# Kernel tuning notes

Measured on AMD Instinct MI355X. Metric: run time of the kernel, lower is better.

The kernel has to match this reference:

```python
import jax, jax.numpy as jnp
import numpy as np

NUM_HEADS = 12
WINDOW = 7            # window_size (and window_pretrain)
MASK_WINDOWS = 64     # windows per image (56x56 feature map / 7x7 windows)
TABLE_SIZE = (2 * WINDOW - 1) ** 2  # 169


def setup_inputs() -> dict:
    key = jax.random.key(0)
    ks = jax.random.split(key, 8)
    B, L, C = 2048, WINDOW * WINDOW, 384
    x = jax.random.normal(ks[0], (B, L, C), jnp.float32)
    rel_index = jax.random.randint(ks[1], (L * L,), 0, TABLE_SIZE, jnp.int32)
    attn_mask = jax.random.normal(ks[2], (1, MASK_WINDOWS, 1, L, L), jnp.float32) * 0.05
    # learned params
    qkv_w = jax.random.normal(ks[3], (C, 3 * C), jnp.float32) * 0.02
    qkv_b = jnp.zeros((3 * C,), jnp.float32)
    rel_bias_table = jax.random.normal(ks[4], (TABLE_SIZE, NUM_HEADS), jnp.float32) * 0.02
    proj_w = jax.random.normal(ks[5], (C, C), jnp.float32) * 0.02
    proj_b = jnp.zeros((C,), jnp.float32)
    return {"x": x, "rel_index": rel_index, "attn_mask": attn_mask,
            "qkv_w": qkv_w, "qkv_b": qkv_b, "rel_bias_table": rel_bias_table,
            "proj_w": proj_w, "proj_b": proj_b}


def reference(x, rel_index, attn_mask, qkv_w, qkv_b, rel_bias_table, proj_w, proj_b):
    B, L, C = x.shape
    H = NUM_HEADS
    D = C // H
    scale = D ** -0.5
    # qkv projection -> [3, B, H, L, D]
    qkv = (x @ qkv_w + qkv_b).reshape(B, L, 3, H, D).transpose(2, 0, 3, 1, 4)
    q, k, v = qkv[0], qkv[1], qkv[2]
    attn = jnp.einsum('bhqd,bhkd->bhqk', q * scale, k)  # [B,H,L,L]
    # gathered relative position bias: [L*L, H] -> [H, L, L]
    bias = rel_bias_table[rel_index].reshape(L, L, H).transpose(2, 0, 1)
    attn = attn + bias[None]
    # shifted-window mask add (with_mask=True path)
    attn = attn.reshape(-1, MASK_WINDOWS, H, L, L) + attn_mask
    attn = attn.reshape(-1, H, L, L)
    attn = jax.nn.softmax(attn, axis=-1)
    out = jnp.einsum('bhqk,bhkd->bqhd', attn, v).reshape(B, L, C)
    return out @ proj_w + proj_b
```

## Files before the change

kernel.cpp:

```cpp
#include <hip/hip_runtime.h>

typedef _Float16 half8 __attribute__((ext_vector_type(8)));
typedef float f32x4 __attribute__((ext_vector_type(4)));

constexpr int NB = 2048;
constexpr int CDIM = 384;
constexpr int NH = 12;
constexpr int MM = NB * 49;
constexpr int NTOT = 1152;
constexpr float SCALE = 0.17677669529663687f;

constexpr int XBLK = 37632;
constexpr int WBLK = 2304;

__device__ __forceinline__ void async16(const void* g, void* l) {
    __builtin_amdgcn_global_load_lds((const __attribute__((address_space(1))) void*)g,
                                     (__attribute__((address_space(3))) void*)l, 16, 0, 0);
}


__global__ __launch_bounds__(256) void prep(const float* __restrict__ x,
                                            const float* __restrict__ qkv_w,
                                            const float* __restrict__ proj_w,
                                            const int* __restrict__ rel_index,
                                            const float* __restrict__ rtable,
                                            const float* __restrict__ mask,
                                            _Float16* __restrict__ x_h,
                                            _Float16* __restrict__ qkvT,
                                            _Float16* __restrict__ projT,
                                            float* __restrict__ FT) {
    int bid = blockIdx.x;
    if (bid < XBLK) {
        size_t i = ((size_t)bid * 256 + threadIdx.x) * 4;
        float4 v = *(const float4*)(x + i);
        _Float16 h0 = (_Float16)v.x, h1 = (_Float16)v.y, h2 = (_Float16)v.z, h3 = (_Float16)v.w;
        _Float16* o = x_h + i;
        o[0] = h0; o[1] = h1; o[2] = h2; o[3] = h3;
    } else if (bid < XBLK + WBLK) {
        int i = (bid - XBLK) * 256 + threadIdx.x;
        if (i < 1152 * 384) {
            int n = i / 384, kk = i % 384;
            qkvT[i] = (_Float16)qkv_w[kk * 1152 + n];
        } else {
            int j = i - 1152 * 384;
            int n = j / 384, kk = j % 384;
            projT[j] = (_Float16)proj_w[kk * 384 + n];
        }
    } else {
        int wh = bid - XBLK - WBLK;
        int w = wh / 12, h = wh - w * 12;
        float* dst = FT + (size_t)wh * 4096;
        for (int idx = threadIdx.x; idx < 4096; idx += 256) {
            int k = idx >> 6, q = idx & 63;
            float v = 0.f;
            if (k < 49 && q < 49)
                v = rtable[rel_index[q * 49 + k] * NH + h] + mask[(size_t)w * 2401 + q * 49 + k];
            dst[idx] = v;
        }
    }
}


__global__ __launch_bounds__(256) void gemm_qkv(const _Float16* __restrict__ A,
                                                const _Float16* __restrict__ Bt,
                                                const float* __restrict__ qkv_b,
                                                _Float16* __restrict__ C) {
    __shared__ union {
        struct { _Float16 A[128 * 64]; _Float16 B[128 * 64]; } st;
        _Float16 tile[128 * 136];
    } sm;
    _Float16* As = sm.st.A;
    _Float16* Bs = sm.st.B;

    const int K = 384;
    const int tn = blockIdx.x, tm = blockIdx.y;
    const int t = threadIdx.x;
    const int wave = t >> 6, lane = t & 63;
    const int wm = (wave & 1) * 64, wn = (wave >> 1) * 64;
    const int quad = lane >> 4, l16 = lane & 15;
    const int rsub = lane >> 3, p = lane & 7;

    f32x4 acc[4][4] = {};
    const _Float16* Abase = A + (size_t)(tm * 128) * K;
    const _Float16* Bbase = Bt + (size_t)(tn * 128) * K;

    for (int k0 = 0; k0 < K; k0 += 64) {
        __syncthreads();
#pragma unroll
        for (int n = 0; n < 4; n++) {
            int ni = wave * 4 + n;
            int row = ni * 8 + rsub;
            int chunk = p ^ (row & 7);
            async16(Abase + (size_t)row * K + k0 + chunk * 8, (char*)As + ni * 1024);
            async16(Bbase + (size_t)row * K + k0 + chunk * 8, (char*)Bs + ni * 1024);
        }
        __syncthreads();
#pragma unroll
        for (int ks = 0; ks < 2; ks++) {
            half8 af[4], bfv[4];
#pragma unroll
            for (int i = 0; i < 4; i++)
                af[i] = *(const half8*)(&As[(wm + i * 16 + l16) * 64 + (((ks * 4 + quad) ^ (l16 & 7)) * 8)]);
#pragma unroll
            for (int j = 0; j < 4; j++)
                bfv[j] = *(const half8*)(&Bs[(wn + j * 16 + l16) * 64 + (((ks * 4 + quad) ^ (l16 & 7)) * 8)]);
#pragma unroll
            for (int i = 0; i < 4; i++)
#pragma unroll
                for (int j = 0; j < 4; j++)
                    acc[i][j] = __builtin_amdgcn_mfma_f32_16x16x32_f16(af[i], bfv[j], acc[i][j], 0, 0, 0);
        }
    }

    __syncthreads();
    const int nbase = tn * 128, mbase = tm * 128;
    const float s = (tn < 3) ? SCALE : 1.f;
    float bj[4];
#pragma unroll
    for (int j = 0; j < 4; j++) bj[j] = qkv_b[nbase + wn + j * 16 + l16];

#pragma unroll
    for (int j = 0; j < 4; j++) {
        int n = wn + j * 16 + l16;
#pragma unroll
        for (int i = 0; i < 4; i++) {
#pragma unroll
            for (int r = 0; r < 4; r++) {
                int m = wm + i * 16 + quad * 4 + r;
                sm.tile[m * 136 + n] = (_Float16)((acc[i][j][r] + bj[j]) * s);
            }
        }
    }
    __syncthreads();

    const int rcol = (t & 15) * 8;
    const int rrow0 = t >> 4;
#pragma unroll
    for (int g = 0; g < 8; g++) {
        int row = g * 16 + rrow0;
        half8 val = *(const half8*)(&sm.tile[row * 136 + rcol]);
        *(half8*)(C + (size_t)(mbase + row) * NTOT + nbase + rcol) = val;
    }
}


__global__ __launch_bounds__(256) void attn_kernel(const _Float16* __restrict__ C,
                                                   const float* __restrict__ FT,
                                                   _Float16* __restrict__ out) {
    __shared__ _Float16 Vt[4][32 * 72];
    __shared__ _Float16 Pb[4][16 * 72];
    const int t = threadIdx.x;
    const int wave = t >> 6, lane = t & 63, quad = lane >> 4, l16 = lane & 15;
    const int gw = blockIdx.x * 4 + wave;
    const int b = gw / 12, h = gw - b * 12;

    const _Float16* qb = C + (size_t)b * 49 * NTOT + h * 32;
    const _Float16* kb = qb + 384;
    const _Float16* vb = qb + 768;
    const float* Fb = FT + ((size_t)((b & 63) * 12 + h)) * 4096;

    _Float16* vt = Vt[wave];
    {
        int d = lane >> 1, seg = lane & 1;
        half8 z = {};
        *(half8*)(&vt[d * 72 + 48 + seg * 8]) = z;
    }
#pragma unroll
    for (int i2 = 0; i2 < 4; i2++) {
        int l = i2 * 16 + (lane >> 2);
        int d0 = (lane & 3) * 8;
        if (l < 49) {
            half8 v8 = *(const half8*)(vb + (size_t)l * NTOT + d0);
#pragma unroll
            for (int e = 0; e < 8; e++)
                vt[(d0 + e) * 72 + l] = v8[e];
        }
    }

    half8 bk[4];
#pragma unroll
    for (int j = 0; j < 4; j++) {
        int krow = j * 16 + l16; if (krow > 48) krow = 48;
        bk[j] = *(const half8*)(kb + (size_t)krow * NTOT + quad * 8);
    }
    half8 bv[2][2];
#pragma unroll
    for (int nt = 0; nt < 2; nt++)
#pragma unroll
        for (int ks = 0; ks < 2; ks++)
            bv[nt][ks] = *(const half8*)(&vt[(nt * 16 + l16) * 72 + ks * 32 + quad * 8]);

    _Float16* Pw = Pb[wave];
#pragma unroll
    for (int i = 0; i < 4; i++) {
        int qrow = i * 16 + l16; if (qrow > 48) qrow = 48;
        half8 aq = *(const half8*)(qb + (size_t)qrow * NTOT + quad * 8);

        f32x4 acc[4];
#pragma unroll
        for (int j = 0; j < 4; j++)
            acc[j] = *(const f32x4*)(Fb + (j * 16 + l16) * 64 + i * 16 + quad * 4);
#pragma unroll
        for (int j = 0; j < 4; j++)
            acc[j] = __builtin_amdgcn_mfma_f32_16x16x32_f16(aq, bk[j], acc[j], 0, 0, 0);

        if (l16 != 0) {
#pragma unroll
            for (int r = 0; r < 4; r++) acc[3][r] = -1e30f;
        }

        float rinv[4];
#pragma unroll
        for (int r = 0; r < 4; r++) {
            float m = fmaxf(fmaxf(acc[0][r], acc[1][r]), fmaxf(acc[2][r], acc[3][r]));
            m = fmaxf(m, __shfl_xor(m, 1, 64));
            m = fmaxf(m, __shfl_xor(m, 2, 64));
            m = fmaxf(m, __shfl_xor(m, 4, 64));
            m = fmaxf(m, __shfl_xor(m, 8, 64));
            float sum = 0.f;
#pragma unroll
            for (int j = 0; j < 4; j++) {
                float e = __expf(acc[j][r] - m);
                acc[j][r] = e;
                sum += e;
            }
            sum += __shfl_xor(sum, 1, 64);
            sum += __shfl_xor(sum, 2, 64);
            sum += __shfl_xor(sum, 4, 64);
            sum += __shfl_xor(sum, 8, 64);
            rinv[r] = 1.f / sum;
        }

#pragma unroll
        for (int j = 0; j < 4; j++)
#pragma unroll
            for (int r = 0; r < 4; r++)
                Pw[(quad * 4 + r) * 72 + j * 16 + l16] = (_Float16)acc[j][r];

        f32x4 oacc[2] = {};
#pragma unroll
        for (int ks = 0; ks < 2; ks++) {
            half8 ap = *(const half8*)(&Pw[l16 * 72 + ks * 32 + quad * 8]);
#pragma unroll
            for (int nt = 0; nt < 2; nt++)
                oacc[nt] = __builtin_amdgcn_mfma_f32_16x16x32_f16(ap, bv[nt][ks], oacc[nt], 0, 0, 0);
        }

#pragma unroll
        for (int nt = 0; nt < 2; nt++)
#pragma unroll
            for (int r = 0; r < 4; r++) {
                int q = i * 16 + quad * 4 + r;
                if (q < 49)
                    out[((size_t)b * 49 + q) * CDIM + h * 32 + nt * 16 + l16] =
                        (_Float16)(oacc[nt][r] * rinv[r]);
            }
    }
}


__global__ __launch_bounds__(256) void gemm_proj(const _Float16* __restrict__ A,
                                                 const _Float16* __restrict__ Bt,
                                                 const float* __restrict__ proj_b,
                                                 float* __restrict__ out) {
    __shared__ _Float16 As[128 * 64];
    __shared__ _Float16 Bs[128 * 64];
    const int K = 384;
    const int tn = blockIdx.x, tm = blockIdx.y;
    const int t = threadIdx.x;
    const int wave = t >> 6, lane = t & 63;
    const int wm = (wave & 1) * 64, wn = (wave >> 1) * 64;
    const int quad = lane >> 4, l16 = lane & 15;
    const int rsub = lane >> 3, p = lane & 7;

    f32x4 acc[4][4] = {};
    const _Float16* Abase = A + (size_t)(tm * 128) * K;
    const _Float16* Bbase = Bt + (size_t)(tn * 128) * K;

    for (int k0 = 0; k0 < K; k0 += 64) {
        __syncthreads();
#pragma unroll
        for (int n = 0; n < 4; n++) {
            int ni = wave * 4 + n;
            int row = ni * 8 + rsub;
            int chunk = p ^ (row & 7);
            async16(Abase + (size_t)row * K + k0 + chunk * 8, (char*)As + ni * 1024);
            async16(Bbase + (size_t)row * K + k0 + chunk * 8, (char*)Bs + ni * 1024);
        }
        __syncthreads();
#pragma unroll
        for (int ks = 0; ks < 2; ks++) {
            half8 af[4], bfv[4];
#pragma unroll
            for (int i = 0; i < 4; i++)
                af[i] = *(const half8*)(&As[(wm + i * 16 + l16) * 64 + (((ks * 4 + quad) ^ (l16 & 7)) * 8)]);
#pragma unroll
            for (int j = 0; j < 4; j++)
                bfv[j] = *(const half8*)(&Bs[(wn + j * 16 + l16) * 64 + (((ks * 4 + quad) ^ (l16 & 7)) * 8)]);
#pragma unroll
            for (int i = 0; i < 4; i++)
#pragma unroll
                for (int j = 0; j < 4; j++)
                    acc[i][j] = __builtin_amdgcn_mfma_f32_16x16x32_f16(af[i], bfv[j], acc[i][j], 0, 0, 0);
        }
    }

    const int mbase = tm * 128, nbase = tn * 128;
#pragma unroll
    for (int j = 0; j < 4; j++) {
        int n = nbase + wn + j * 16 + l16;
        float bias = proj_b[n];
#pragma unroll
        for (int i = 0; i < 4; i++) {
#pragma unroll
            for (int r = 0; r < 4; r++) {
                int m = mbase + wm + i * 16 + quad * 4 + r;
                out[(size_t)m * CDIM + n] = acc[i][j][r] + bias;
            }
        }
    }
}


extern "C" void kernel_launch(void* const* d_in, const int* in_sizes, int n_in,
                              void* d_out, int out_size, void* d_ws, size_t ws_size,
                              hipStream_t stream) {
    const float* x        = (const float*)d_in[0];
    const int*   rel_idx  = (const int*)d_in[1];
    const float* amask    = (const float*)d_in[2];
    const float* qkv_w    = (const float*)d_in[3];
    const float* qkv_b    = (const float*)d_in[4];
    const float* rtable   = (const float*)d_in[5];
    const float* proj_w   = (const float*)d_in[6];
    const float* proj_b   = (const float*)d_in[7];
    float* out = (float*)d_out;

    char* w = (char*)d_ws;
    const size_t XB = (size_t)MM * CDIM * 2;
    const size_t CB = (size_t)MM * NTOT * 2;
    _Float16* x_h    = (_Float16*)w;
    _Float16* wqkvT  = (_Float16*)(w + XB);
    _Float16* wprojT = (_Float16*)(w + XB + 884736);
    _Float16* Cbuf   = (_Float16*)(w + XB + 884736 + 294912);
    float*    FT     = (float*)(w + XB + 884736 + 294912 + CB);
    _Float16* ao_h   = x_h;

    prep<<<XBLK + WBLK + 768, 256, 0, stream>>>(x, qkv_w, proj_w, rel_idx, rtable, amask,
                                                x_h, wqkvT, wprojT, FT);
    gemm_qkv<<<dim3(9, MM / 128), 256, 0, stream>>>(x_h, wqkvT, qkv_b, Cbuf);
    attn_kernel<<<NB * NH / 4, 256, 0, stream>>>(Cbuf, FT, ao_h);
    gemm_proj<<<dim3(3, MM / 128), 256, 0, stream>>>(ao_h, wprojT, proj_b, out);
}
```

Baseline: 625.8 us.

## Fuse QKV projection with window attention per window, remap proj GEMM blocks

Replaces the separate QKV GEMM and attention kernels with one kernel per window. It loads the 49x384 input tile into LDS, computes Q/K/V for three heads per wave pair with MFMA, and runs softmax attention directly from LDS. This removes the round trip of the large fp16 QKV intermediate through global memory. The cost is that weights are read from global/L2 per window with low reuse, LDS use is high, and the padded 64-row tile reads past the last window (handled by padding the workspace). The projection GEMM also gets a 1D grid with a chunked block remap, probably for XCD/L2 locality.

```diff
diff --git a/kernel.cpp b/kernel.cpp
--- a/kernel.cpp
+++ b/kernel.cpp
@@ -7,11 +7,13 @@
 constexpr int CDIM = 384;
 constexpr int NH = 12;
 constexpr int MM = NB * 49;
-constexpr int NTOT = 1152;
 constexpr float SCALE = 0.17677669529663687f;
 
 constexpr int XBLK = 37632;
 constexpr int WBLK = 2304;
+
+constexpr int PROJ_BLOCKS = 3 * (MM / 128);
+constexpr int PROJ_CHUNK  = PROJ_BLOCKS / 8;
 
 __device__ __forceinline__ void async16(const void* g, void* l) {
     __builtin_amdgcn_global_load_lds((const __attribute__((address_space(1))) void*)g,
@@ -61,200 +63,158 @@
 }
 
 
-__global__ __launch_bounds__(256) void gemm_qkv(const _Float16* __restrict__ A,
-                                                const _Float16* __restrict__ Bt,
-                                                const float* __restrict__ qkv_b,
-                                                _Float16* __restrict__ C) {
-    __shared__ union {
-        struct { _Float16 A[128 * 64]; _Float16 B[128 * 64]; } st;
-        _Float16 tile[128 * 136];
-    } sm;
-    _Float16* As = sm.st.A;
-    _Float16* Bs = sm.st.B;
-
-    const int K = 384;
-    const int tn = blockIdx.x, tm = blockIdx.y;
+__global__ __launch_bounds__(512, 2) void qkv_attn(const _Float16* __restrict__ x_h,
+                                                   const _Float16* __restrict__ qkvT,
+                                                   const float* __restrict__ qkv_b,
+                                                   const float* __restrict__ FT,
+                                                   _Float16* __restrict__ ao) {
+    __shared__ _Float16 xs[64 * 384];
+    __shared__ _Float16 Qs[4][64 * 40];
+    __shared__ _Float16 Ks[4][64 * 40];
+    __shared__ _Float16 Vt[4][32 * 72];
+    __shared__ _Float16 Pb[8][16 * 72];
+
+    const int b = blockIdx.x;
     const int t = threadIdx.x;
     const int wave = t >> 6, lane = t & 63;
-    const int wm = (wave & 1) * 64, wn = (wave >> 1) * 64;
     const int quad = lane >> 4, l16 = lane & 15;
-    const int rsub = lane >> 3, p = lane & 7;
-
-    f32x4 acc[4][4] = {};
-    const _Float16* Abase = A + (size_t)(tm * 128) * K;
-    const _Float16* Bbase = Bt + (size_t)(tn * 128) * K;
-
-    for (int k0 = 0; k0 < K; k0 += 64) {
+    const int gsel = wave >> 1, p = wave & 1;
+
+    const _Float16* xw = x_h + (size_t)b * 49 * 384;
+#pragma unroll
+    for (int rnd = 0; rnd < 6; rnd++) {
+        int g = rnd * 512 + t;
+        int row = g / 48, c = g - row * 48;
+        int cs = c ^ (row & 7);
+        async16(xw + row * 384 + cs * 8, (char*)xs + (rnd * 8192 + wave * 1024));
+    }
+    __syncthreads();
+
+    _Float16* Qg = Qs[gsel];
+    _Float16* Kg = Ks[gsel];
+    _Float16* Vg = Vt[gsel];
+    _Float16* Pw = Pb[wave];
+
+    for (int hi = 0; hi < 3; hi++) {
+        const int h = gsel * 3 + hi;
+        const int col = p * 16 + l16;
+        const _Float16* wq = qkvT + (size_t)(h * 32 + col) * 384;
+        const _Float16* wk = wq + (size_t)384 * 384;
+        const _Float16* wv = wk + (size_t)384 * 384;
+        const float bq_b = qkv_b[h * 32 + col];
+        const float bk_b = qkv_b[384 + h * 32 + col];
+        const float bv_b = qkv_b[768 + h * 32 + col];
+
+        f32x4 qa[4] = {}, ka[4] = {}, va[4] = {};
+#pragma unroll
+        for (int kk = 0; kk < 12; kk++) {
+            half8 a[4];
+#pragma unroll
+            for (int i = 0; i < 4; i++) {
+                int row = i * 16 + l16;
+                a[i] = *(const half8*)(&xs[row * 384 + (((kk * 4 + quad) ^ (row & 7)) * 8)]);
+            }
+            half8 bq = *(const half8*)(wq + kk * 32 + quad * 8);
+            half8 bk = *(const half8*)(wk + kk * 32 + quad * 8);
+            half8 bv = *(const half8*)(wv + kk * 32 + quad * 8);
+#pragma unroll
+            for (int i = 0; i < 4; i++) {
+                qa[i] = __builtin_amdgcn_mfma_f32_16x16x32_f16(a[i], bq, qa[i], 0, 0, 0);
+                ka[i] = __builtin_amdgcn_mfma_f32_16x16x32_f16(a[i], bk, ka[i], 0, 0, 0);
+                va[i] = __builtin_amdgcn_mfma_f32_16x16x32_f16(a[i], bv, va[i], 0, 0, 0);
+            }
+        }
+
+        if (hi > 0) __syncthreads();
+
+#pragma unroll
+        for (int i = 0; i < 4; i++) {
+#pragma unroll
+            for (int r = 0; r < 4; r++) {
+                int row = i * 16 + quad * 4 + r;
+                Qg[row * 40 + col] = (_Float16)((qa[i][r] + bq_b) * SCALE);
+                Kg[row * 40 + col] = (_Float16)(ka[i][r] + bk_b);
+                Vg[col * 72 + row] = (row < 49) ? (_Float16)(va[i][r] + bv_b) : (_Float16)0.f;
+            }
+        }
         __syncthreads();
-#pragma unroll
-        for (int n = 0; n < 4; n++) {
-            int ni = wave * 4 + n;
-            int row = ni * 8 + rsub;
-            int chunk = p ^ (row & 7);
-            async16(Abase + (size_t)row * K + k0 + chunk * 8, (char*)As + ni * 1024);
-            async16(Bbase + (size_t)row * K + k0 + chunk * 8, (char*)Bs + ni * 1024);
-        }
-        __syncthreads();
-#pragma unroll
-        for (int ks = 0; ks < 2; ks++) {
-            half8 af[4], bfv[4];
-#pragma unroll
-            for (int i = 0; i < 4; i++)
-                af[i] = *(const half8*)(&As[(wm + i * 16 + l16) * 64 + (((ks * 4 + quad) ^ (l16 & 7)) * 8)]);
+
+        const float* Fb = FT + ((size_t)((b & 63) * 12 + h)) * 4096;
+        half8 bkf[4];
+#pragma unroll
+        for (int j = 0; j < 4; j++)
+            bkf[j] = *(const half8*)(&Kg[(j * 16 + l16) * 40 + quad * 8]);
+        half8 bvf[2][2];
+#pragma unroll
+        for (int nt = 0; nt < 2; nt++)
+#pragma unroll
+            for (int k2 = 0; k2 < 2; k2++)
+                bvf[nt][k2] = *(const half8*)(&Vg[(nt * 16 + l16) * 72 + k2 * 32 + quad * 8]);
+
+#pragma unroll
+        for (int i2 = 0; i2 < 2; i2++) {
+            const int i = p * 2 + i2;
+            half8 aq = *(const half8*)(&Qg[(i * 16 + l16) * 40 + quad * 8]);
+            f32x4 acc[4];
 #pragma unroll
             for (int j = 0; j < 4; j++)
-                bfv[j] = *(const half8*)(&Bs[(wn + j * 16 + l16) * 64 + (((ks * 4 + quad) ^ (l16 & 7)) * 8)]);
-#pragma unroll
-            for (int i = 0; i < 4; i++)
-#pragma unroll
-                for (int j = 0; j < 4; j++)
-                    acc[i][j] = __builtin_amdgcn_mfma_f32_16x16x32_f16(af[i], bfv[j], acc[i][j], 0, 0, 0);
-        }
-    }
-
-    __syncthreads();
-    const int nbase = tn * 128, mbase = tm * 128;
-    const float s = (tn < 3) ? SCALE : 1.f;
-    float bj[4];
-#pragma unroll
-    for (int j = 0; j < 4; j++) bj[j] = qkv_b[nbase + wn + j * 16 + l16];
-
-#pragma unroll
-    for (int j = 0; j < 4; j++) {
-        int n = wn + j * 16 + l16;
-#pragma unroll
-        for (int i = 0; i < 4; i++) {
+                acc[j] = *(const f32x4*)(Fb + (j * 16 + l16) * 64 + i * 16 + quad * 4);
+#pragma unroll
+            for (int j = 0; j < 4; j++)
+                acc[j] = __builtin_amdgcn_mfma_f32_16x16x32_f16(aq, bkf[j], acc[j], 0, 0, 0);
+
+            if (l16 != 0) {
+#pragma unroll
+                for (int r = 0; r < 4; r++) acc[3][r] = -1e30f;
+            }
+
+            float rinv[4];
 #pragma unroll
             for (int r = 0; r < 4; r++) {
-                int m = wm + i * 16 + quad * 4 + r;
-                sm.tile[m * 136 + n] = (_Float16)((acc[i][j][r] + bj[j]) * s);
-            }
-        }
-    }
-    __syncthreads();
-
-    const int rcol = (t & 15) * 8;
-    const int rrow0 = t >> 4;
-#pragma unroll
-    for (int g = 0; g < 8; g++) {
-        int row = g * 16 + rrow0;
-        half8 val = *(const half8*)(&sm.tile[row * 136 + rcol]);
-        *(half8*)(C + (size_t)(mbase + row) * NTOT + nbase + rcol) = val;
-    }
-}
-
-
-__global__ __launch_bounds__(256) void attn_kernel(const _Float16* __restrict__ C,
-                                                   const float* __restrict__ FT,
-                                                   _Float16* __restrict__ out) {
-    __shared__ _Float16 Vt[4][32 * 72];
-    __shared__ _Float16 Pb[4][16 * 72];
-    const int t = threadIdx.x;
-    const int wave = t >> 6, lane = t & 63, quad = lane >> 4, l16 = lane & 15;
-    const int gw = blockIdx.x * 4 + wave;
-    const int b = gw / 12, h = gw - b * 12;
-
-    const _Float16* qb = C + (size_t)b * 49 * NTOT + h * 32;
-    const _Float16* kb = qb + 384;
-    const _Float16* vb = qb + 768;
-    const float* Fb = FT + ((size_t)((b & 63) * 12 + h)) * 4096;
-
-    _Float16* vt = Vt[wave];
-    {
-        int d = lane >> 1, seg = lane & 1;
-        half8 z = {};
-        *(half8*)(&vt[d * 72 + 48 + seg * 8]) = z;
-    }
-#pragma unroll
-    for (int i2 = 0; i2 < 4; i2++) {
-        int l = i2 * 16 + (lane >> 2);
-        int d0 = (lane & 3) * 8;
-        if (l < 49) {
-            half8 v8 = *(const half8*)(vb + (size_t)l * NTOT + d0);
-#pragma unroll
-            for (int e = 0; e < 8; e++)
-                vt[(d0 + e) * 72 + l] = v8[e];
-        }
-    }
-
-    half8 bk[4];
-#pragma unroll
-    for (int j = 0; j < 4; j++) {
-        int krow = j * 16 + l16; if (krow > 48) krow = 48;
-        bk[j] = *(const half8*)(kb + (size_t)krow * NTOT + quad * 8);
-    }
-    half8 bv[2][2];
-#pragma unroll
-    for (int nt = 0; nt < 2; nt++)
-#pragma unroll
-        for (int ks = 0; ks < 2; ks++)
-            bv[nt][ks] = *(const half8*)(&vt[(nt * 16 + l16) * 72 + ks * 32 + quad * 8]);
-
-    _Float16* Pw = Pb[wave];
-#pragma unroll
-    for (int i = 0; i < 4; i++) {
-        int qrow = i * 16 + l16; if (qrow > 48) qrow = 48;
-        half8 aq = *(const half8*)(qb + (size_t)qrow * NTOT + quad * 8);
-
-        f32x4 acc[4];
-#pragma unroll
-        for (int j = 0; j < 4; j++)
-            acc[j] = *(const f32x4*)(Fb + (j * 16 + l16) * 64 + i * 16 + quad * 4);
-#pragma unroll
-        for (int j = 0; j < 4; j++)
-            acc[j] = __builtin_amdgcn_mfma_f32_16x16x32_f16(aq, bk[j], acc[j], 0, 0, 0);
-
-        if (l16 != 0) {
-#pragma unroll
-            for (int r = 0; r < 4; r++) acc[3][r] = -1e30f;
-        }
-
-        float rinv[4];
-#pragma unroll
-        for (int r = 0; r < 4; r++) {
-            float m = fmaxf(fmaxf(acc[0][r], acc[1][r]), fmaxf(acc[2][r], acc[3][r]));
-            m = fmaxf(m, __shfl_xor(m, 1, 64));
-            m = fmaxf(m, __shfl_xor(m, 2, 64));
-            m = fmaxf(m, __shfl_xor(m, 4, 64));
-            m = fmaxf(m, __shfl_xor(m, 8, 64));
-            float sum = 0.f;
-#pragma unroll
-            for (int j = 0; j < 4; j++) {
-                float e = __expf(acc[j][r] - m);
-                acc[j][r] = e;
-                sum += e;
-            }
-            sum += __shfl_xor(sum, 1, 64);
-            sum += __shfl_xor(sum, 2, 64);
-            sum += __shfl_xor(sum, 4, 64);
-            sum += __shfl_xor(sum, 8, 64);
-            rinv[r] = 1.f / sum;
-        }
-
-#pragma unroll
-        for (int j = 0; j < 4; j++)
-#pragma unroll
-            for (int r = 0; r < 4; r++)
-                Pw[(quad * 4 + r) * 72 + j * 16 + l16] = (_Float16)acc[j][r];
-
-        f32x4 oacc[2] = {};
-#pragma unroll
-        for (int ks = 0; ks < 2; ks++) {
-            half8 ap = *(const half8*)(&Pw[l16 * 72 + ks * 32 + quad * 8]);
+                float m = fmaxf(fmaxf(acc[0][r], acc[1][r]), fmaxf(acc[2][r], acc[3][r]));
+                m = fmaxf(m, __shfl_xor(m, 1, 64));
+                m = fmaxf(m, __shfl_xor(m, 2, 64));
+                m = fmaxf(m, __shfl_xor(m, 4, 64));
+                m = fmaxf(m, __shfl_xor(m, 8, 64));
+                float sum = 0.f;
+#pragma unroll
+                for (int j = 0; j < 4; j++) {
+                    float e = __expf(acc[j][r] - m);
+                    acc[j][r] = e;
+                    sum += e;
+                }
+                sum += __shfl_xor(sum, 1, 64);
+                sum += __shfl_xor(sum, 2, 64);
+                sum += __shfl_xor(sum, 4, 64);
+                sum += __shfl_xor(sum, 8, 64);
+                rinv[r] = 1.f / sum;
+            }
+
+#pragma unroll
+            for (int j = 0; j < 4; j++)
+#pragma unroll
+                for (int r = 0; r < 4; r++)
+                    Pw[(quad * 4 + r) * 72 + j * 16 + l16] = (_Float16)acc[j][r];
+
+            f32x4 oacc[2] = {};
+#pragma unroll
+            for (int k2 = 0; k2 < 2; k2++) {
+                half8 ap = *(const half8*)(&Pw[l16 * 72 + k2 * 32 + quad * 8]);
+#pragma unroll
+                for (int nt = 0; nt < 2; nt++)
+                    oacc[nt] = __builtin_amdgcn_mfma_f32_16x16x32_f16(ap, bvf[nt][k2], oacc[nt], 0, 0, 0);
+            }
+
 #pragma unroll
             for (int nt = 0; nt < 2; nt++)
-                oacc[nt] = __builtin_amdgcn_mfma_f32_16x16x32_f16(ap, bv[nt][ks], oacc[nt], 0, 0, 0);
-        }
-
-#pragma unroll
-        for (int nt = 0; nt < 2; nt++)
-#pragma unroll
-            for (int r = 0; r < 4; r++) {
-                int q = i * 16 + quad * 4 + r;
-                if (q < 49)
-                    out[((size_t)b * 49 + q) * CDIM + h * 32 + nt * 16 + l16] =
-                        (_Float16)(oacc[nt][r] * rinv[r]);
-            }
+#pragma unroll
+                for (int r = 0; r < 4; r++) {
+                    int q = i * 16 + quad * 4 + r;
+                    if (q < 49)
+                        ao[((size_t)b * 49 + q) * CDIM + h * 32 + nt * 16 + l16] =
+                            (_Float16)(oacc[nt][r] * rinv[r]);
+                }
+        }
     }
 }
 
@@ -266,12 +226,14 @@
     __shared__ _Float16 As[128 * 64];
     __shared__ _Float16 Bs[128 * 64];
     const int K = 384;
-    const int tn = blockIdx.x, tm = blockIdx.y;
+    const int bid = blockIdx.x;
+    const int wid = (bid & 7) * PROJ_CHUNK + (bid >> 3);
+    const int tn = wid % 3, tm = wid / 3;
     const int t = threadIdx.x;
     const int wave = t >> 6, lane = t & 63;
     const int wm = (wave & 1) * 64, wn = (wave >> 1) * 64;
     const int quad = lane >> 4, l16 = lane & 15;
-    const int rsub = lane >> 3, p = lane & 7;
+    const int rsub = lane >> 3, pp = lane & 7;
 
     f32x4 acc[4][4] = {};
     const _Float16* Abase = A + (size_t)(tm * 128) * K;
@@ -283,7 +245,7 @@
         for (int n = 0; n < 4; n++) {
             int ni = wave * 4 + n;
             int row = ni * 8 + rsub;
-            int chunk = p ^ (row & 7);
+            int chunk = pp ^ (row & 7);
             async16(Abase + (size_t)row * K + k0 + chunk * 8, (char*)As + ni * 1024);
             async16(Bbase + (size_t)row * K + k0 + chunk * 8, (char*)Bs + ni * 1024);
         }
@@ -336,18 +298,16 @@
     float* out = (float*)d_out;
 
     char* w = (char*)d_ws;
-    const size_t XB = (size_t)MM * CDIM * 2;
-    const size_t CB = (size_t)MM * NTOT * 2;
+    const size_t XB  = (size_t)MM * CDIM * 2;
+    const size_t XBP = XB + 12288;
     _Float16* x_h    = (_Float16*)w;
-    _Float16* wqkvT  = (_Float16*)(w + XB);
-    _Float16* wprojT = (_Float16*)(w + XB + 884736);
-    _Float16* Cbuf   = (_Float16*)(w + XB + 884736 + 294912);
-    float*    FT     = (float*)(w + XB + 884736 + 294912 + CB);
-    _Float16* ao_h   = x_h;
+    _Float16* wqkvT  = (_Float16*)(w + XBP);
+    _Float16* wprojT = (_Float16*)(w + XBP + 884736);
+    float*    FT     = (float*)(w + XBP + 884736 + 294912);
+    _Float16* ao_h   = (_Float16*)(w + XBP + 884736 + 294912 + 12582912);
 
     prep<<<XBLK + WBLK + 768, 256, 0, stream>>>(x, qkv_w, proj_w, rel_idx, rtable, amask,
                                                 x_h, wqkvT, wprojT, FT);
-    gemm_qkv<<<dim3(9, MM / 128), 256, 0, stream>>>(x_h, wqkvT, qkv_b, Cbuf);
-    attn_kernel<<<NB * NH / 4, 256, 0, stream>>>(Cbuf, FT, ao_h);
-    gemm_proj<<<dim3(3, MM / 128), 256, 0, stream>>>(ao_h, wprojT, proj_b, out);
-}
+    qkv_attn<<<NB, 512, 0, stream>>>(x_h, wqkvT, qkv_b, FT, ao_h);
+    gemm_proj<<<PROJ_BLOCKS, 256, 0, stream>>>(ao_h, wprojT, proj_b, out);
+}
```

After: 664.7 us. 1.06x slower.
